# Optimization experiments

Hardware: AMD Instinct MI355X
Metric: run time of the kernel (lower is better)

## Reference

```python
import jax, jax.numpy as jnp
import numpy as np

B, S, E, NH = 2, 1024, 2048, 16
DH = E // NH
EPS = 1e-6

def setup_inputs() -> dict:
    key = jax.random.key(0)
    ks = jax.random.split(key, 6)
    q = jax.random.normal(ks[0], (B, S, E), dtype=jnp.float32)
    k = jax.random.normal(ks[1], (B, S, E), dtype=jnp.float32)
    v = jax.random.normal(ks[2], (B, S, E), dtype=jnp.float32)
    Wi = jax.random.normal(ks[3], (3 * E, NH), dtype=jnp.float32) * 0.02
    bi = jax.random.normal(ks[4], (NH,), dtype=jnp.float32) * 0.1
    Wf = jax.random.normal(ks[5], (3 * E, NH), dtype=jnp.float32) * 0.02
    bf = jnp.linspace(3.0, 6.0, NH, dtype=jnp.float32)  # bias_linspace_initializer(3,6)
    ln_scale = jnp.ones((E,), dtype=jnp.float32)
    return {"q": q, "k": k, "v": v, "Wi": Wi, "bi": bi, "Wf": Wf, "bf": bf, "ln_scale": ln_scale}

def _mlstm_forward(q, k, v, Wi, bi, Wf, bf, ln_scale):
    b, s, e = q.shape
    nh = Wi.shape[1]
    dh = e // nh
    x = jnp.concatenate([q, k, v], axis=-1)                     # (B,S,3E)
    ig = (x @ Wi + bi).transpose(0, 2, 1)[..., None]            # (B,NH,S,1)
    fg = (x @ Wf + bf).transpose(0, 2, 1)[..., None]            # (B,NH,S,1)
    split = lambda t: t.reshape(b, s, nh, dh).transpose(0, 2, 1, 3)
    qh, kh, vh = split(q), split(k), split(v)                   # (B,NH,S,DH)
    # parallel_stabilized_simple backend
    log_f = jax.nn.log_sigmoid(fg)                              # (B,NH,S,1)
    log_f_cum = jnp.concatenate(
        [jnp.zeros((b, nh, 1, 1), q.dtype), jnp.cumsum(log_f, axis=2)], axis=2
    )                                                           # (B,NH,S+1,1)
    # D[i,j] = cumsum[i] - cumsum[j] on causal part
    fg_mat = log_f_cum - jnp.transpose(log_f_cum, (0, 1, 3, 2)) # (B,NH,S+1,S+1)
    ltr = jnp.tril(jnp.ones((s, s), dtype=bool))
    log_fg = jnp.where(ltr, fg_mat[:, :, 1:, 1:], -jnp.inf)     # (B,NH,S,S)
    log_D = log_fg + jnp.transpose(ig, (0, 1, 3, 2))            # + i_j per column
    max_log_D = jnp.max(log_D, axis=-1, keepdims=True)          # (B,NH,S,1)
    D = jnp.exp(log_D - max_log_D)
    qk = jnp.einsum('bhsd,bhtd->bhst', qh, kh) / jnp.sqrt(jnp.asarray(dh, q.dtype))
    C = qk * D                                                  # (B,NH,S,S)
    normalizer = jnp.maximum(jnp.abs(C.sum(-1, keepdims=True)), jnp.exp(-max_log_D))
    Cn = C / (normalizer + EPS)
    h = jnp.einsum('bhst,bhtd->bhsd', Cn, vh)                   # (B,NH,S,DH)
    # MultiHeadLayerNorm: normalize over DH per head, scale (no bias)
    mu = h.mean(-1, keepdims=True)
    var = ((h - mu) ** 2).mean(-1, keepdims=True)
    hn = (h - mu) * jax.lax.rsqrt(var + EPS)
    hn = hn * ln_scale.reshape(1, nh, 1, dh)
    return hn.transpose(0, 2, 1, 3).reshape(b, s, e)            # (B,S,E)

def reference(q, k, v, Wi, bi, Wf, bf, ln_scale):
    return _mlstm_forward(q, k, v, Wi, bi, Wf, bf, ln_scale)
```

## Files before the change

kernel.cpp:

```cpp
#include <hip/hip_runtime.h>
#include <hip/hip_bf16.h>

#define B_   2
#define S_   1024
#define E_   2048
#define NH_  16
#define DH_  128
#define EPS_ 1e-6f

using half8   = __attribute__((ext_vector_type(8))) _Float16;
using floatx4 = __attribute__((ext_vector_type(4))) float;

__device__ __forceinline__ half8 cvt8h(const float* __restrict__ p) {
    float4 a = *(const float4*)p;
    float4 b = *(const float4*)(p + 4);
    half8 r;
    r[0] = (_Float16)a.x; r[1] = (_Float16)a.y;
    r[2] = (_Float16)a.z; r[3] = (_Float16)a.w;
    r[4] = (_Float16)b.x; r[5] = (_Float16)b.y;
    r[6] = (_Float16)b.z; r[7] = (_Float16)b.w;
    return r;
}

__global__ __launch_bounds__(256, 2) void prep_kernel(
    const float* __restrict__ q, const float* __restrict__ k,
    const float* __restrict__ v, _Float16* __restrict__ qh,
    _Float16* __restrict__ kh, _Float16* __restrict__ vtg)
{
    __shared__ __attribute__((aligned(16))) _Float16 vs[64 * 136];
    const int t  = threadIdx.x;
    const int st = blockIdx.x, bh = blockIdx.y;
    const int b  = bh >> 4, h = bh & 15;
    const int s0 = st * 64;
    const int r  = t >> 2, d0 = (t & 3) * 32;
    const size_t gin  = ((size_t)b * S_ + s0 + r) * E_ + h * DH_ + d0;
    const size_t gout = ((size_t)bh * S_ + s0 + r) * DH_ + d0;
    #pragma unroll
    for (int i = 0; i < 4; ++i)
        *(half8*)(qh + gout + i * 8) = cvt8h(q + gin + i * 8);
    #pragma unroll
    for (int i = 0; i < 4; ++i)
        *(half8*)(kh + gout + i * 8) = cvt8h(k + gin + i * 8);
    #pragma unroll
    for (int i = 0; i < 4; ++i)
        *(half8*)(&vs[r * 136 + d0 + i * 8]) = cvt8h(v + gin + i * 8);
    __syncthreads();
    const int d = t >> 1, j0 = (t & 1) * 32;
    _Float16 tmp[32];
    #pragma unroll
    for (int jj = 0; jj < 32; ++jj)
        tmp[jj] = vs[(j0 + jj) * 136 + d];
    const size_t vout = ((size_t)bh * DH_ + d) * S_ + s0 + j0;
    #pragma unroll
    for (int i = 0; i < 4; ++i)
        *(half8*)(vtg + vout + i * 8) = *(half8*)(&tmp[i * 8]);
}

__global__ __launch_bounds__(256, 4) void gates_kernel(
    const float* __restrict__ q, const float* __restrict__ k,
    const float* __restrict__ v, const float* __restrict__ Wi,
    const float* __restrict__ Wf, float* __restrict__ pre_i,
    float* __restrict__ pre_f)
{
    __shared__ __attribute__((aligned(16))) _Float16 xs[32 * 264];
    __shared__ __attribute__((aligned(16))) _Float16 wt[32 * 264];

    const int t    = threadIdx.x;
    const int w    = t >> 6, lane = t & 63, quad = lane >> 4, l15 = lane & 15;
    const int mw   = w & 1, nw = w >> 1;
    const int m0   = blockIdx.x * 32;
    const int by   = blockIdx.y;
    const int kbase = by * 768;

    floatx4 acc = {0.f, 0.f, 0.f, 0.f};

    for (int c = 0; c < 3; ++c) {
        __syncthreads();
        const int e0   = kbase + c * 256;
        const int tsel = e0 >> 11;
        const int el0  = e0 & 2047;
        const float* xb = (tsel == 0) ? q : (tsel == 1) ? k : v;
        #pragma unroll
        for (int i = 0; i < 4; ++i) {
            int g = t + i * 256;
            int row = g >> 5, grp = g & 31;
            half8 s8 = cvt8h(xb + (size_t)(m0 + row) * E_ + el0 + grp * 8);
            *(half8*)(&xs[row * 264 + grp * 8]) = s8;
        }
        {
            const int kk = t;
            const float* wiRow = Wi + (size_t)(e0 + kk) * NH_;
            const float* wfRow = Wf + (size_t)(e0 + kk) * NH_;
            float wif[16], wff[16];
            #pragma unroll
            for (int i4 = 0; i4 < 4; ++i4) {
                float4 a = *(const float4*)(wiRow + i4 * 4);
                wif[i4*4+0]=a.x; wif[i4*4+1]=a.y; wif[i4*4+2]=a.z; wif[i4*4+3]=a.w;
                float4 b = *(const float4*)(wfRow + i4 * 4);
                wff[i4*4+0]=b.x; wff[i4*4+1]=b.y; wff[i4*4+2]=b.z; wff[i4*4+3]=b.w;
            }
            #pragma unroll
            for (int hh = 0; hh < 16; ++hh) wt[hh * 264 + kk]        = (_Float16)wif[hh];
            #pragma unroll
            for (int hh = 0; hh < 16; ++hh) wt[(16 + hh) * 264 + kk] = (_Float16)wff[hh];
        }
        __syncthreads();
        #pragma unroll
        for (int ks = 0; ks < 8; ++ks) {
            half8 af = *(const half8*)(&xs[(mw * 16 + l15) * 264 + ks * 32 + quad * 8]);
            half8 bw = *(const half8*)(&wt[(nw * 16 + l15) * 264 + ks * 32 + quad * 8]);
            acc = __builtin_amdgcn_mfma_f32_16x16x32_f16(af, bw, acc, 0, 0, 0);
        }
    }
    #pragma unroll
    for (int reg = 0; reg < 4; ++reg) {
        int m   = m0 + mw * 16 + quad * 4 + reg;
        int b   = m >> 10, s = m & 1023;
        int col = nw * 16 + l15;
        float vacc = acc[reg];
        if (col < 16)
            pre_i[((size_t)(by * 32 + b * NH_ + col)) * S_ + s] = vacc;
        else
            pre_f[((size_t)(by * 32 + b * NH_ + col - 16)) * S_ + s] = vacc;
    }
}

__global__ __launch_bounds__(1024, 1) void scan_kernel(
    const float* __restrict__ pre_i, const float* __restrict__ pre_f,
    float* __restrict__ Aj, float* __restrict__ Cq,
    float* __restrict__ NFo, const float* __restrict__ bi,
    const float* __restrict__ bfb)
{
    __shared__ float wsumF[16], wmaxA[16];
    const int bh   = blockIdx.x;
    const int h    = bh & 15;
    const int t    = threadIdx.x;
    const int lane = t & 63, wv = t >> 6;

    float igv = bi[h], x = bfb[h];
    #pragma unroll
    for (int y = 0; y < 8; ++y) {
        igv += pre_i[((size_t)(y * 32 + bh)) * S_ + t];
        x   += pre_f[((size_t)(y * 32 + bh)) * S_ + t];
    }
    float lfv = (x >= 0.f) ? -log1pf(__expf(-x)) : (x - log1pf(__expf(x)));

    float sc = lfv;
    #pragma unroll
    for (int off = 1; off < 64; off <<= 1) {
        float o = __shfl_up(sc, off);
        if (lane >= off) sc += o;
    }
    if (lane == 63) wsumF[wv] = sc;
    __syncthreads();
    float Foff = 0.f;
    for (int i = 0; i < wv; ++i) Foff += wsumF[i];
    float F = Foff + sc;
    float a = igv - F;

    float ms = a;
    #pragma unroll
    for (int off = 1; off < 64; off <<= 1) {
        float o = __shfl_up(ms, off);
        if (lane >= off) ms = fmaxf(ms, o);
    }
    if (lane == 63) wmaxA[wv] = ms;
    __syncthreads();
    float Moff = -3.0e38f;
    for (int i = 0; i < wv; ++i) Moff = fmaxf(Moff, wmaxA[i]);
    float M = fmaxf(Moff, ms);

    size_t o = (size_t)bh * S_ + t;
    Aj[o]  = a;
    Cq[o]  = -M;
    NFo[o] = expf(fminf(-(F + M), 80.f));
}

__global__ __launch_bounds__(256, 2) void attn_kernel(
    const _Float16* __restrict__ qh, const _Float16* __restrict__ kh,
    const _Float16* __restrict__ vtg, const float* __restrict__ Aj,
    const float* __restrict__ Cq, const float* __restrict__ NFi,
    const float* __restrict__ lnsc, float* __restrict__ out)
{
    __shared__ __attribute__((aligned(16))) _Float16 Ks[64 * 136];
    __shared__ __attribute__((aligned(16))) _Float16 Vt[128 * 72];
    __shared__ __attribute__((aligned(16))) _Float16 Pb[64 * 72];
    __shared__ float aj[64];

    const int t    = threadIdx.x;
    const int w    = t >> 6, lane = t & 63, quad = lane >> 4, l15 = lane & 15;
    const int L    = blockIdx.x;
    int qi, bh;
    if (L < 256) { qi = L >> 5;                bh = L & 31; }
    else         { qi = 15 - ((L - 256) >> 5); bh = (L - 256) & 31; }
    const int b    = bh >> 4, h = bh & 15;
    const int q0   = qi * 64;
    const int krow = t >> 2, kd0 = (t & 3) * 32;
    const int vd   = t >> 1, vj0 = (t & 1) * 32;

    float ci_r[4], nfv_r[4];
    #pragma unroll
    for (int reg = 0; reg < 4; ++reg) {
        int rl = w * 16 + quad * 4 + reg;
        ci_r[reg]  = Cq[(size_t)bh * S_ + q0 + rl];
        nfv_r[reg] = NFi[(size_t)bh * S_ + q0 + rl];
    }
    half8 aq[4];
    {
        const _Float16* qrow = qh + ((size_t)bh * S_ + q0 + w * 16 + l15) * DH_;
        #pragma unroll
        for (int ks = 0; ks < 4; ++ks)
            aq[ks] = *(const half8*)(qrow + ks * 32 + quad * 8);
    }

    half8 kreg[4], vreg[4];
    float ajreg = 0.f;
    {
        const _Float16* kp = kh + ((size_t)bh * S_ + krow) * DH_ + kd0;
        const _Float16* vp = vtg + ((size_t)bh * DH_ + vd) * S_ + vj0;
        #pragma unroll
        for (int i = 0; i < 4; ++i) { kreg[i] = *(const half8*)(kp + i * 8);
                                      vreg[i] = *(const half8*)(vp + i * 8); }
    }
    if (t < 64) ajreg = Aj[(size_t)bh * S_ + t];

    #pragma unroll
    for (int i = 0; i < 4; ++i) {
        *(half8*)(&Ks[krow * 136 + kd0 + i * 8]) = kreg[i];
        *(half8*)(&Vt[vd * 72 + vj0 + i * 8])    = vreg[i];
    }
    if (t < 64) aj[t] = ajreg;
    __syncthreads();

    floatx4 acc_h[8];
    #pragma unroll
    for (int i = 0; i < 8; ++i) acc_h[i] = (floatx4){0.f, 0.f, 0.f, 0.f};
    float lrun[4] = {0.f, 0.f, 0.f, 0.f};
    const float rscale = 0.08838834764831845f;

    for (int kt = 0; kt <= qi; ++kt) {
        if (kt < qi) {
            const int j0n = (kt + 1) * 64;
            const _Float16* kp = kh + ((size_t)bh * S_ + j0n + krow) * DH_ + kd0;
            const _Float16* vp = vtg + ((size_t)bh * DH_ + vd) * S_ + j0n + vj0;
            #pragma unroll
            for (int i = 0; i < 4; ++i) { kreg[i] = *(const half8*)(kp + i * 8);
                                          vreg[i] = *(const half8*)(vp + i * 8); }
            if (t < 64) ajreg = Aj[(size_t)bh * S_ + j0n + t];
        }

        floatx4 sacc[4];
        #pragma unroll
        for (int nt = 0; nt < 4; ++nt) sacc[nt] = (floatx4){0.f, 0.f, 0.f, 0.f};
        #pragma unroll
        for (int ks = 0; ks < 4; ++ks) {
            #pragma unroll
            for (int nt = 0; nt < 4; ++nt) {
                half8 bk = *(const half8*)(&Ks[(nt * 16 + l15) * 136 + ks * 32 + quad * 8]);
                sacc[nt] = __builtin_amdgcn_mfma_f32_16x16x32_f16(aq[ks], bk, sacc[nt], 0, 0, 0);
            }
        }
        const bool diag = (kt == qi);
        #pragma unroll
        for (int nt = 0; nt < 4; ++nt) {
            int jl = nt * 16 + l15;
            float a_j = aj[jl];
            #pragma unroll
            for (int reg = 0; reg < 4; ++reg) {
                int rl = w * 16 + quad * 4 + reg;
                float p = 0.f;
                if (!diag || (jl <= rl))
                    p = sacc[nt][reg] * rscale * __expf(fminf(ci_r[reg] + a_j, 0.f));
                lrun[reg] += p;
                Pb[rl * 72 + jl] = (_Float16)p;
            }
        }
        #pragma unroll
        for (int ks2 = 0; ks2 < 2; ++ks2) {
            half8 ap = *(const half8*)(&Pb[(w * 16 + l15) * 72 + ks2 * 32 + quad * 8]);
            #pragma unroll
            for (int nt2 = 0; nt2 < 8; ++nt2) {
                half8 bv = *(const half8*)(&Vt[(nt2 * 16 + l15) * 72 + ks2 * 32 + quad * 8]);
                acc_h[nt2] = __builtin_amdgcn_mfma_f32_16x16x32_f16(ap, bv, acc_h[nt2], 0, 0, 0);
            }
        }

        __syncthreads();
        if (kt < qi) {
            #pragma unroll
            for (int i = 0; i < 4; ++i) {
                *(half8*)(&Ks[krow * 136 + kd0 + i * 8]) = kreg[i];
                *(half8*)(&Vt[vd * 72 + vj0 + i * 8])    = vreg[i];
            }
            if (t < 64) aj[t] = ajreg;
            __syncthreads();
        }
    }

    #pragma unroll
    for (int reg = 0; reg < 4; ++reg) {
        float l = lrun[reg];
        #pragma unroll
        for (int off = 1; off < 16; off <<= 1) l += __shfl_xor(l, off);
        int rl = w * 16 + quad * 4 + reg;
        float nrm = fmaxf(fabsf(l), nfv_r[reg]) + EPS_;
        float inv = 1.f / nrm;
        float hv[8];
        float sum = 0.f, sq = 0.f;
        #pragma unroll
        for (int nt2 = 0; nt2 < 8; ++nt2) {
            float x = acc_h[nt2][reg] * inv;
            hv[nt2] = x; sum += x; sq += x * x;
        }
        #pragma unroll
        for (int off = 1; off < 16; off <<= 1) {
            sum += __shfl_xor(sum, off);
            sq  += __shfl_xor(sq, off);
        }
        float mean = sum * (1.f / 128.f);
        float var  = fmaxf(sq * (1.f / 128.f) - mean * mean, 0.f);
        float rstd = rsqrtf(var + EPS_);
        size_t orow = ((size_t)b * S_ + q0 + rl) * E_ + h * DH_;
        #pragma unroll
        for (int nt2 = 0; nt2 < 8; ++nt2) {
            int d = nt2 * 16 + l15;
            out[orow + d] = (hv[nt2] - mean) * rstd * lnsc[h * DH_ + d];
        }
    }
}

extern "C" void kernel_launch(void* const* d_in, const int* in_sizes, int n_in,
                              void* d_out, int out_size, void* d_ws, size_t ws_size,
                              hipStream_t stream)
{
    const float* q    = (const float*)d_in[0];
    const float* k    = (const float*)d_in[1];
    const float* v    = (const float*)d_in[2];
    const float* Wi   = (const float*)d_in[3];
    const float* bi   = (const float*)d_in[4];
    const float* Wf   = (const float*)d_in[5];
    const float* bfb  = (const float*)d_in[6];
    const float* lnsc = (const float*)d_in[7];
    float* out        = (float*)d_out;

    const int NS  = B_ * NH_ * S_;
    float* pre_i = (float*)d_ws;
    float* pre_f = pre_i + 8 * NS;
    float* Aj    = pre_f + 8 * NS;
    float* Cq    = Aj + NS;
    float* NFa   = Cq + NS;
    _Float16* qh  = (_Float16*)(NFa + NS);
    _Float16* kh  = qh + (size_t)32 * S_ * DH_;
    _Float16* vtg = kh + (size_t)32 * S_ * DH_;

    prep_kernel<<<dim3(16, 32), 256, 0, stream>>>(q, k, v, qh, kh, vtg);
    gates_kernel<<<dim3(64, 8), 256, 0, stream>>>(q, k, v, Wi, Wf, pre_i, pre_f);
    scan_kernel<<<dim3(32), 1024, 0, stream>>>(pre_i, pre_f, Aj, Cq, NFa, bi, bfb);
    attn_kernel<<<dim3(512), 256, 0, stream>>>(qh, kh, vtg, Aj, Cq, NFa, lnsc, out);
}
```

Before: 161.7 us.

## Fuse fp16 q/k/v conversion and V transpose into gates kernel

Removes the separate prep kernel and has the gates GEMM kernel write the fp16 head-split q and k tiles, plus a transposed fp16 V, from the shared-memory tiles it already loads. This avoids a second full read of q, k and v from global memory and one kernel launch. The cost is extra global stores and a strided LDS column read inside the gates kernel, which may lengthen that kernel and raise bank conflicts.

```diff
diff --git a/kernel.cpp b/kernel.cpp
--- a/kernel.cpp
+++ b/kernel.cpp
@@ -22,45 +22,12 @@
     return r;
 }
 
-__global__ __launch_bounds__(256, 2) void prep_kernel(
-    const float* __restrict__ q, const float* __restrict__ k,
-    const float* __restrict__ v, _Float16* __restrict__ qh,
-    _Float16* __restrict__ kh, _Float16* __restrict__ vtg)
-{
-    __shared__ __attribute__((aligned(16))) _Float16 vs[64 * 136];
-    const int t  = threadIdx.x;
-    const int st = blockIdx.x, bh = blockIdx.y;
-    const int b  = bh >> 4, h = bh & 15;
-    const int s0 = st * 64;
-    const int r  = t >> 2, d0 = (t & 3) * 32;
-    const size_t gin  = ((size_t)b * S_ + s0 + r) * E_ + h * DH_ + d0;
-    const size_t gout = ((size_t)bh * S_ + s0 + r) * DH_ + d0;
-    #pragma unroll
-    for (int i = 0; i < 4; ++i)
-        *(half8*)(qh + gout + i * 8) = cvt8h(q + gin + i * 8);
-    #pragma unroll
-    for (int i = 0; i < 4; ++i)
-        *(half8*)(kh + gout + i * 8) = cvt8h(k + gin + i * 8);
-    #pragma unroll
-    for (int i = 0; i < 4; ++i)
-        *(half8*)(&vs[r * 136 + d0 + i * 8]) = cvt8h(v + gin + i * 8);
-    __syncthreads();
-    const int d = t >> 1, j0 = (t & 1) * 32;
-    _Float16 tmp[32];
-    #pragma unroll
-    for (int jj = 0; jj < 32; ++jj)
-        tmp[jj] = vs[(j0 + jj) * 136 + d];
-    const size_t vout = ((size_t)bh * DH_ + d) * S_ + s0 + j0;
-    #pragma unroll
-    for (int i = 0; i < 4; ++i)
-        *(half8*)(vtg + vout + i * 8) = *(half8*)(&tmp[i * 8]);
-}
-
 __global__ __launch_bounds__(256, 4) void gates_kernel(
     const float* __restrict__ q, const float* __restrict__ k,
     const float* __restrict__ v, const float* __restrict__ Wi,
     const float* __restrict__ Wf, float* __restrict__ pre_i,
-    float* __restrict__ pre_f)
+    float* __restrict__ pre_f, _Float16* __restrict__ qhg,
+    _Float16* __restrict__ khg, _Float16* __restrict__ vtg)
 {
     __shared__ __attribute__((aligned(16))) _Float16 xs[32 * 264];
     __shared__ __attribute__((aligned(16))) _Float16 wt[32 * 264];
@@ -71,6 +38,8 @@
     const int m0   = blockIdx.x * 32;
     const int by   = blockIdx.y;
     const int kbase = by * 768;
+    const int bblk = m0 >> 10;
+    const int s0   = m0 & 1023;
 
     floatx4 acc = {0.f, 0.f, 0.f, 0.f};
 
@@ -80,12 +49,18 @@
         const int tsel = e0 >> 11;
         const int el0  = e0 & 2047;
         const float* xb = (tsel == 0) ? q : (tsel == 1) ? k : v;
+        _Float16* fout = (tsel == 0) ? qhg : khg;
         #pragma unroll
         for (int i = 0; i < 4; ++i) {
             int g = t + i * 256;
             int row = g >> 5, grp = g & 31;
             half8 s8 = cvt8h(xb + (size_t)(m0 + row) * E_ + el0 + grp * 8);
             *(half8*)(&xs[row * 264 + grp * 8]) = s8;
+            if (tsel < 2) {
+                int el = el0 + grp * 8;
+                int h  = el >> 7, d = el & 127;
+                *(half8*)(fout + ((size_t)(bblk * NH_ + h) * S_ + s0 + row) * DH_ + d) = s8;
+            }
         }
         {
             const int kk = t;
@@ -105,6 +80,18 @@
             for (int hh = 0; hh < 16; ++hh) wt[(16 + hh) * 264 + kk] = (_Float16)wff[hh];
         }
         __syncthreads();
+        if (tsel == 2) {
+            const int col = t;
+            const int el  = el0 + col;
+            const int h   = el >> 7, d = el & 127;
+            _Float16 tmp[32];
+            #pragma unroll
+            for (int r = 0; r < 32; ++r) tmp[r] = xs[r * 264 + col];
+            const size_t vo = ((size_t)(bblk * NH_ + h) * DH_ + d) * S_ + s0;
+            #pragma unroll
+            for (int i = 0; i < 4; ++i)
+                *(half8*)(vtg + vo + i * 8) = *(half8*)(&tmp[i * 8]);
+        }
         #pragma unroll
         for (int ks = 0; ks < 8; ++ks) {
             half8 af = *(const half8*)(&xs[(mw * 16 + l15) * 264 + ks * 32 + quad * 8]);
@@ -353,8 +340,8 @@
     _Float16* kh  = qh + (size_t)32 * S_ * DH_;
     _Float16* vtg = kh + (size_t)32 * S_ * DH_;
 
-    prep_kernel<<<dim3(16, 32), 256, 0, stream>>>(q, k, v, qh, kh, vtg);
-    gates_kernel<<<dim3(64, 8), 256, 0, stream>>>(q, k, v, Wi, Wf, pre_i, pre_f);
+    gates_kernel<<<dim3(64, 8), 256, 0, stream>>>(q, k, v, Wi, Wf, pre_i, pre_f,
+                                                  qh, kh, vtg);
     scan_kernel<<<dim3(32), 1024, 0, stream>>>(pre_i, pre_f, Aj, Cq, NFa, bi, bfb);
     attn_kernel<<<dim3(512), 256, 0, stream>>>(qh, kh, vtg, Aj, Cq, NFa, lnsc, out);
 }
```

After: 149.1 us. 7.8% less time.
